# Kernel tuning notes

Hardware: AMD Instinct MI355X
Metric: run time of the kernel (lower is better)

The kernel has to match this reference:

```python
import jax, jax.numpy as jnp
import numpy as np

HIDDEN = 4096
NUM_HEADS = 32
HEAD_DIM = HIDDEN // NUM_HEADS  # 128
ROPE_THETA = 10000.0
SCALE = HEAD_DIM ** -0.5


def _apply_rope_neox(x, positions):
    # x: [B, S, H, D], positions: [B, S] int
    half = HEAD_DIM // 2
    inv_freq = 1.0 / (ROPE_THETA ** (jnp.arange(0, half, dtype=jnp.float32) / half))
    freqs = positions.astype(jnp.float32)[..., None] * inv_freq  # [B, S, half]
    cos = jnp.cos(freqs)[:, :, None, :]  # [B, S, 1, half]
    sin = jnp.sin(freqs)[:, :, None, :]
    x1, x2 = x[..., :half], x[..., half:]
    return jnp.concatenate([x1 * cos - x2 * sin, x2 * cos + x1 * sin], axis=-1)


def setup_inputs() -> dict:
    key = jax.random.key(0)
    k1, k2, k3, k4 = jax.random.split(key, 4)
    B, S = 2, 2048
    positions = jnp.broadcast_to(jnp.arange(S, dtype=jnp.int32), (B, S))
    hidden_states = jax.random.normal(k1, (B, S, HIDDEN), dtype=jnp.float32)
    w_qkv = jax.random.normal(k2, (HIDDEN, 3 * HIDDEN), dtype=jnp.float32) * (HIDDEN ** -0.5)
    b_qkv = jax.random.normal(k3, (3 * HIDDEN,), dtype=jnp.float32) * 0.02
    w_proj = jax.random.normal(k4, (HIDDEN, HIDDEN), dtype=jnp.float32) * (HIDDEN ** -0.5)
    return {"positions": positions, "hidden_states": hidden_states,
            "w_qkv": w_qkv, "b_qkv": b_qkv, "w_proj": w_proj}


def reference(positions, hidden_states, w_qkv, b_qkv, w_proj):
    B, S, _ = hidden_states.shape
    qkv = hidden_states @ w_qkv + b_qkv                     # [B, S, 3*HIDDEN]
    q, k, v = jnp.split(qkv, 3, axis=-1)
    q = q.reshape(B, S, NUM_HEADS, HEAD_DIM)
    k = k.reshape(B, S, NUM_HEADS, HEAD_DIM)
    v = v.reshape(B, S, NUM_HEADS, HEAD_DIM)
    q = _apply_rope_neox(q, positions)
    k = _apply_rope_neox(k, positions)
    scores = jnp.einsum('bqhd,bkhd->bhqk', q, k) * SCALE    # [B, H, S, S]
    causal = jnp.tril(jnp.ones((S, S), dtype=bool))
    scores = jnp.where(causal, scores, jnp.finfo(scores.dtype).min)
    probs = jax.nn.softmax(scores, axis=-1)
    attn = jnp.einsum('bhqk,bkhd->bqhd', probs, v).reshape(B, S, HIDDEN)
    return attn @ w_proj
```

## Files before the change

### kernel.cpp

```cpp
#include <hip/hip_runtime.h>
#include <hip/hip_bf16.h>
#include <math.h>

constexpr int B_   = 2;
constexpr int SEQ  = 2048;
constexpr int HID  = 4096;
constexpr int NH   = 32;
constexpr int HD   = 128;
constexpr float SCALE = 0.08838834764831845f;
constexpr size_t TEN = (size_t)B_ * NH * SEQ * HD;

typedef __attribute__((ext_vector_type(8))) __bf16 bf16x8;
typedef __attribute__((ext_vector_type(4))) float f32x4;

__device__ __forceinline__ ushort f2bf(float f) {
  uint u = __float_as_uint(f);
  return (ushort)((u + 0x7fffu + ((u >> 16) & 1u)) >> 16);
}
__device__ __forceinline__ float bfl(uint u) { return __uint_as_float(u << 16); }

__device__ __forceinline__ void gload16(const void* g, void* l) {
  __builtin_amdgcn_global_load_lds((__attribute__((address_space(1))) void*)(g),
                                   (__attribute__((address_space(3))) void*)(l),
                                   16, 0, 0);
}

__global__ __launch_bounds__(256) void conv_bf16(const float* __restrict__ in,
                                                 ushort* __restrict__ out) {
  const size_t i = ((size_t)blockIdx.x * 256 + threadIdx.x) * 8;
  float4 x = *(const float4*)(in + i);
  float4 y = *(const float4*)(in + i + 4);
  uint4 pk;
  pk.x = (uint)f2bf(x.x) | ((uint)f2bf(x.y) << 16);
  pk.y = (uint)f2bf(x.z) | ((uint)f2bf(x.w) << 16);
  pk.z = (uint)f2bf(y.x) | ((uint)f2bf(y.y) << 16);
  pk.w = (uint)f2bf(y.z) | ((uint)f2bf(y.w) << 16);
  *(uint4*)(out + i) = pk;
}

__global__ __launch_bounds__(256) void transp_bf16(const float* __restrict__ in,
                                                   ushort* __restrict__ out,
                                                   int R, int C) {
  __shared__ float t[32][33];
  const int tx = threadIdx.x & 31, ty = threadIdx.x >> 5;
  const int c0 = blockIdx.x * 32, r0 = blockIdx.y * 32;
  #pragma unroll
  for (int i = 0; i < 4; ++i)
    t[ty + 8*i][tx] = in[(size_t)(r0 + ty + 8*i) * C + c0 + tx];
  __syncthreads();
  #pragma unroll
  for (int i = 0; i < 4; ++i)
    out[(size_t)(c0 + ty + 8*i) * R + r0 + tx] = f2bf(t[tx][ty + 8*i]);
}

template<int MODE>
__global__ __launch_bounds__(256) void gemm_mfma(const ushort* __restrict__ A,
                                                 const ushort* __restrict__ Bt,
                                                 const float* __restrict__ bias,
                                                 void* __restrict__ outp,
                                                 int N, int K) {
  __shared__ __align__(16) ushort As[128 * 32];
  __shared__ __align__(16) ushort Bs[128 * 32];
  const int tid = threadIdx.x;
  const int wave = tid >> 6, lane = tid & 63;
  const int wr = wave >> 1, wc = wave & 1;
  const int m0 = blockIdx.y * 128, n0 = blockIdx.x * 128;

  f32x4 acc[4][4];
  #pragma unroll
  for (int i = 0; i < 4; ++i)
    #pragma unroll
    for (int j = 0; j < 4; ++j) acc[i][j] = (f32x4){0.f, 0.f, 0.f, 0.f};

  const int srow = 32 * wave + (lane >> 2);
  const int skq8 = (lane & 3) * 8;
  const ushort* Ag0 = A  + (size_t)(m0 + srow) * K + skq8;
  const ushort* Bg0 = Bt + (size_t)(n0 + srow) * K + skq8;
  char* AsB = (char*)As + wave * 2048;
  char* BsB = (char*)Bs + wave * 2048;

  const int fl  = lane & 15;
  const int kh8 = (lane >> 4) * 8;
  const ushort* Ar = As + (wr * 64 + fl) * 32 + kh8;
  const ushort* Br = Bs + (wc * 64 + fl) * 32 + kh8;

  for (int k0 = 0; k0 < K; k0 += 32) {
    __syncthreads();
    gload16(Ag0 + k0,          AsB);
    gload16(Ag0 + k0 + 16 * K, AsB + 1024);
    gload16(Bg0 + k0,          BsB);
    gload16(Bg0 + k0 + 16 * K, BsB + 1024);
    __syncthreads();
    bf16x8 a[4], b[4];
    #pragma unroll
    for (int m = 0; m < 4; ++m) a[m] = *(const bf16x8*)(Ar + m * 512);
    #pragma unroll
    for (int n = 0; n < 4; ++n) b[n] = *(const bf16x8*)(Br + n * 512);
    #pragma unroll
    for (int m = 0; m < 4; ++m)
      #pragma unroll
      for (int n = 0; n < 4; ++n)
        acc[m][n] = __builtin_amdgcn_mfma_f32_16x16x32_bf16(a[m], b[n], acc[m][n], 0, 0, 0);
  }

  const int rq4 = (lane >> 4) * 4;
  if (MODE == 0) {
    const int which = n0 >> 12;
    const int h     = (n0 >> 7) & 31;
    ushort* dst0 = (ushort*)outp + (size_t)which * TEN + (size_t)h * (SEQ * HD);
    #pragma unroll
    for (int n = 0; n < 4; ++n) {
      const int d = wc * 64 + n * 16 + fl;
      const float bv = bias[n0 + d];
      #pragma unroll
      for (int m = 0; m < 4; ++m) {
        const int rowb = m0 + wr * 64 + m * 16 + rq4;
        #pragma unroll
        for (int r = 0; r < 4; ++r) {
          const int t = rowb + r;
          const int b = t >> 11, s = t & 2047;
          dst0[(size_t)b * (NH * SEQ * HD) + (size_t)s * HD + d] = f2bf(acc[m][n][r] + bv);
        }
      }
    }
  } else {
    float* C = (float*)outp;
    #pragma unroll
    for (int n = 0; n < 4; ++n) {
      const int d = wc * 64 + n * 16 + fl;
      #pragma unroll
      for (int m = 0; m < 4; ++m) {
        const int rowb = m0 + wr * 64 + m * 16 + rq4;
        #pragma unroll
        for (int r = 0; r < 4; ++r)
          C[(size_t)(rowb + r) * N + n0 + d] = acc[m][n][r];
      }
    }
  }
}

__global__ __launch_bounds__(256) void rope_kernel(ushort* __restrict__ qbuf,
                                                   ushort* __restrict__ kbuf,
                                                   const int* __restrict__ positions) {
  const int idx = blockIdx.x * 256 + threadIdx.x;
  const int d  = idx & 63;
  const int s  = (idx >> 6) & 2047;
  const int bh = idx >> 17;
  const size_t off = ((size_t)bh * SEQ + s) * HD;
  const int pos = positions[(bh >> 5) * SEQ + s];
  const float invf = exp2f(-(float)d * 0.20762050593046014f);
  const float ang = (float)pos * invf;
  float sn, cs;
  sincosf(ang, &sn, &cs);
  {
    float x1 = bfl(qbuf[off + d]), x2 = bfl(qbuf[off + d + 64]);
    qbuf[off + d]      = f2bf((x1 * cs - x2 * sn) * SCALE);
    qbuf[off + d + 64] = f2bf((x2 * cs + x1 * sn) * SCALE);
  }
  {
    float x1 = bfl(kbuf[off + d]), x2 = bfl(kbuf[off + d + 64]);
    kbuf[off + d]      = f2bf(x1 * cs - x2 * sn);
    kbuf[off + d + 64] = f2bf(x2 * cs + x1 * sn);
  }
}

__global__ __launch_bounds__(256) void attn_mfma(const ushort* __restrict__ Q,
                                                 const ushort* __restrict__ K,
                                                 const ushort* __restrict__ V,
                                                 ushort* __restrict__ Out) {
  __shared__ __align__(16) ushort Ks[64 * 128];
  __shared__ __align__(16) ushort Vt[128 * 64];
  __shared__ __align__(16) ushort Pl[4 * 16 * 64];
  const int tid  = threadIdx.x;
  const int wave = tid >> 6, lane = tid & 63;
  const int fl = lane & 15, hh = lane >> 4;
  const int qs   = blockIdx.x * 64;
  const int qs_w = qs + wave * 16;
  const int bh   = blockIdx.y;
  const ushort* Qb = Q + (size_t)bh * SEQ * HD;
  const ushort* Kb = K + (size_t)bh * SEQ * HD;
  const ushort* Vb = V + (size_t)bh * SEQ * HD;

  bf16x8 qa[4];
  {
    const ushort* qrow = Qb + (size_t)(qs_w + fl) * HD + hh * 8;
    #pragma unroll
    for (int kk = 0; kk < 4; ++kk)
      qa[kk] = *(const bf16x8*)(qrow + 32 * kk);
  }

  f32x4 o_acc[8];
  #pragma unroll
  for (int dt = 0; dt < 8; ++dt) o_acc[dt] = (f32x4){0.f, 0.f, 0.f, 0.f};
  float mrow[4] = {-INFINITY, -INFINITY, -INFINITY, -INFINITY};
  float lrow[4] = {0.f, 0.f, 0.f, 0.f};

  char* KsC = (char*)Ks;
  char* VtC = (char*)Vt;
  ushort* Pw = Pl + wave * (16 * 64);

  const int nt = qs / 64 + 1;
  for (int jt = 0; jt < nt; ++jt) {
    const int j0 = jt * 64;
    __syncthreads();

    #pragma unroll
    for (int i = 0; i < 4; ++i) {
      const int seg = i * 4 + wave;
      const int row = 4 * seg + hh;
      const int gc  = fl ^ (row & 7);
      gload16(Kb + (size_t)(j0 + row) * HD + gc * 8, KsC + seg * 1024);
    }
    #pragma unroll
    for (int a = 0; a < 2; ++a) {
      const int idx   = tid + a * 256;
      const int chunk = idx & 15;
      const int pair  = idx >> 4;
      const int d0    = chunk * 8;
      uint4 v0 = *(const uint4*)(Vb + (size_t)(j0 + 2 * pair) * HD + d0);
      uint4 v1 = *(const uint4*)(Vb + (size_t)(j0 + 2 * pair + 1) * HD + d0);
      const ushort* u0 = (const ushort*)&v0;
      const ushort* u1 = (const ushort*)&v1;
      #pragma unroll
      for (int j = 0; j < 8; ++j) {
        const int d = d0 + j;
        const int byt = (d * 128 + pair * 4) ^ (((d >> 3) & 7) << 4);
        *(uint*)(VtC + byt) = (uint)u0[j] | ((uint)u1[j] << 16);
      }
    }
    __syncthreads();

    f32x4 sa[4];
    #pragma unroll
    for (int cc = 0; cc < 4; ++cc) sa[cc] = (f32x4){0.f, 0.f, 0.f, 0.f};
    #pragma unroll
    for (int cc = 0; cc < 4; ++cc) {
      const int row = fl + 16 * cc;
      const int rsw = row & 7;
      #pragma unroll
      for (int kk = 0; kk < 4; ++kk) {
        bf16x8 kb = *(const bf16x8*)(KsC + row * 256 + ((hh + 4 * kk) ^ rsw) * 16);
        sa[cc] = __builtin_amdgcn_mfma_f32_16x16x32_bf16(qa[kk], kb, sa[cc], 0, 0, 0);
      }
    }

    if (jt == nt - 1) {
      #pragma unroll
      for (int cc = 0; cc < 4; ++cc) {
        const int kv_g = j0 + fl + 16 * cc;
        #pragma unroll
        for (int r = 0; r < 4; ++r)
          if (kv_g > qs_w + 4 * hh + r) sa[cc][r] = -3.0e38f;
      }
    }

    float tmax[4], psum[4], resc[4];
    #pragma unroll
    for (int r = 0; r < 4; ++r) {
      float t = fmaxf(fmaxf(sa[0][r], sa[1][r]), fmaxf(sa[2][r], sa[3][r]));
      #pragma unroll
      for (int off = 1; off < 16; off <<= 1)
        t = fmaxf(t, __shfl_xor(t, off));
      tmax[r] = t;
    }
    #pragma unroll
    for (int r = 0; r < 4; ++r) {
      const float mnew = fmaxf(mrow[r], tmax[r]);
      resc[r] = __expf(mrow[r] - mnew);
      mrow[r] = mnew;
      float ps = 0.f;
      #pragma unroll
      for (int cc = 0; cc < 4; ++cc) {
        const float p = __expf(sa[cc][r] - mnew);
        sa[cc][r] = p;
        ps += p;
      }
      psum[r] = ps;
    }
    #pragma unroll
    for (int r = 0; r < 4; ++r) {
      float ps = psum[r];
      #pragma unroll
      for (int off = 1; off < 16; off <<= 1)
        ps += __shfl_xor(ps, off);
      lrow[r] = lrow[r] * resc[r] + ps;
    }
    #pragma unroll
    for (int dt = 0; dt < 8; ++dt)
      #pragma unroll
      for (int r = 0; r < 4; ++r) o_acc[dt][r] *= resc[r];

    #pragma unroll
    for (int cc = 0; cc < 4; ++cc) {
      const int kv = fl + 16 * cc;
      #pragma unroll
      for (int r = 0; r < 4; ++r) {
        const int q = 4 * hh + r;
        const int byt = q * 128 + (((kv >> 3) ^ (q & 7)) << 4) + (kv & 7) * 2;
        *(ushort*)((char*)Pw + byt) = f2bf(sa[cc][r]);
      }
    }

    #pragma unroll
    for (int chunk = 0; chunk < 2; ++chunk) {
      bf16x8 pa = *(const bf16x8*)((char*)Pw + fl * 128 +
                                   (((hh + 4 * chunk) ^ (fl & 7)) << 4));
      #pragma unroll
      for (int dt = 0; dt < 8; ++dt) {
        const int d = fl + 16 * dt;
        bf16x8 vbf = *(const bf16x8*)(VtC + ((d * 128 + hh * 16 + 64 * chunk) ^
                                             (((d >> 3) & 7) << 4)));
        o_acc[dt] = __builtin_amdgcn_mfma_f32_16x16x32_bf16(pa, vbf, o_acc[dt], 0, 0, 0);
      }
    }
  }

  float inv[4];
  #pragma unroll
  for (int r = 0; r < 4; ++r) inv[r] = 1.0f / lrow[r];
  const int b = bh >> 5, h = bh & 31;
  #pragma unroll
  for (int dt = 0; dt < 8; ++dt) {
    const int d = h * HD + dt * 16 + fl;
    #pragma unroll
    for (int r = 0; r < 4; ++r) {
      const int row_g = qs_w + 4 * hh + r;
      Out[((size_t)(b * SEQ + row_g)) * HID + d] = f2bf(o_acc[dt][r] * inv[r]);
    }
  }
}

extern "C" void kernel_launch(void* const* d_in, const int* in_sizes, int n_in,
                              void* d_out, int out_size, void* d_ws, size_t ws_size,
                              hipStream_t stream) {
  const int*   positions = (const int*)d_in[0];
  const float* hidden    = (const float*)d_in[1];
  const float* w_qkv     = (const float*)d_in[2];
  const float* b_qkv     = (const float*)d_in[3];
  const float* w_proj    = (const float*)d_in[4];
  float* out = (float*)d_out;

  ushort* ws16 = (ushort*)d_ws;
  ushort* qb = ws16;
  ushort* kb = ws16 + TEN;
  ushort* vb = ws16 + 2 * TEN;
  ushort* wT = ws16 + 3 * TEN;
  ushort* hA = ws16 + 3 * TEN + (size_t)(3 * HID) * HID;

  conv_bf16<<<8192, 256, 0, stream>>>(hidden, hA);
  transp_bf16<<<dim3(3 * HID / 32, HID / 32), 256, 0, stream>>>(w_qkv, wT, HID, 3 * HID);
  gemm_mfma<0><<<dim3(3 * HID / 128, 32), 256, 0, stream>>>(hA, wT, b_qkv, (void*)qb,
                                                            3 * HID, HID);
  rope_kernel<<<32768, 256, 0, stream>>>(qb, kb, positions);
  transp_bf16<<<dim3(HID / 32, HID / 32), 256, 0, stream>>>(w_proj, wT, HID, HID);
  attn_mfma<<<dim3(SEQ / 64, B_ * NH), 256, 0, stream>>>(qb, kb, vb, hA);
  gemm_mfma<1><<<dim3(HID / 128, 32), 256, 0, stream>>>(hA, wT, nullptr, (void*)out,
                                                        HID, HID);
}
```

Baseline: 1.960 ms.

## Double-buffer K/V tiles in attention and schedule longest causal blocks first

The attention kernel now double-buffers the K and V tiles in shared memory. The next tile's K is issued via async global-to-LDS loads and its V is loaded into registers before the current tile is computed, and V is transposed into LDS afterward. This overlaps global memory latency with MFMA work and drops one barrier per iteration. The grid is also reordered so the heaviest causal query blocks launch first, which reduces tail imbalance. The cost is twice the LDS for K/V (lower occupancy possible) and extra registers for the V prefetch.

```diff
diff --git a/kernel.cpp b/kernel.cpp
--- a/kernel.cpp
+++ b/kernel.cpp
@@ -168,15 +168,16 @@
                                                  const ushort* __restrict__ K,
                                                  const ushort* __restrict__ V,
                                                  ushort* __restrict__ Out) {
-  __shared__ __align__(16) ushort Ks[64 * 128];
-  __shared__ __align__(16) ushort Vt[128 * 64];
+  __shared__ __align__(16) ushort Ks[2][64 * 128];
+  __shared__ __align__(16) ushort Vt[2][128 * 64];
   __shared__ __align__(16) ushort Pl[4 * 16 * 64];
   const int tid  = threadIdx.x;
   const int wave = tid >> 6, lane = tid & 63;
   const int fl = lane & 15, hh = lane >> 4;
-  const int qs   = blockIdx.x * 64;
+  const int bh = blockIdx.x;
+  const int qi = (int)gridDim.y - 1 - (int)blockIdx.y;
+  const int qs   = qi * 64;
   const int qs_w = qs + wave * 16;
-  const int bh   = blockIdx.y;
   const ushort* Qb = Q + (size_t)bh * SEQ * HD;
   const ushort* Kb = K + (size_t)bh * SEQ * HD;
   const ushort* Vb = V + (size_t)bh * SEQ * HD;
@@ -195,15 +196,11 @@
   float mrow[4] = {-INFINITY, -INFINITY, -INFINITY, -INFINITY};
   float lrow[4] = {0.f, 0.f, 0.f, 0.f};
 
-  char* KsC = (char*)Ks;
-  char* VtC = (char*)Vt;
   ushort* Pw = Pl + wave * (16 * 64);
-
-  const int nt = qs / 64 + 1;
-  for (int jt = 0; jt < nt; ++jt) {
-    const int j0 = jt * 64;
-    __syncthreads();
-
+  uint4 vreg[4];
+
+  auto stageK = [&](int buf, int j0) {
+    char* KsC = (char*)Ks[buf];
     #pragma unroll
     for (int i = 0; i < 4; ++i) {
       const int seg = i * 4 + wave;
@@ -211,16 +208,26 @@
       const int gc  = fl ^ (row & 7);
       gload16(Kb + (size_t)(j0 + row) * HD + gc * 8, KsC + seg * 1024);
     }
+  };
+  auto loadV = [&](int j0) {
     #pragma unroll
     for (int a = 0; a < 2; ++a) {
-      const int idx   = tid + a * 256;
-      const int chunk = idx & 15;
-      const int pair  = idx >> 4;
-      const int d0    = chunk * 8;
-      uint4 v0 = *(const uint4*)(Vb + (size_t)(j0 + 2 * pair) * HD + d0);
-      uint4 v1 = *(const uint4*)(Vb + (size_t)(j0 + 2 * pair + 1) * HD + d0);
-      const ushort* u0 = (const ushort*)&v0;
-      const ushort* u1 = (const ushort*)&v1;
+      const int idx  = tid + a * 256;
+      const int d0   = (idx & 15) * 8;
+      const int pair = idx >> 4;
+      vreg[2*a]   = *(const uint4*)(Vb + (size_t)(j0 + 2*pair)     * HD + d0);
+      vreg[2*a+1] = *(const uint4*)(Vb + (size_t)(j0 + 2*pair + 1) * HD + d0);
+    }
+  };
+  auto writeV = [&](int buf) {
+    char* VtC = (char*)Vt[buf];
+    #pragma unroll
+    for (int a = 0; a < 2; ++a) {
+      const int idx  = tid + a * 256;
+      const int d0   = (idx & 15) * 8;
+      const int pair = idx >> 4;
+      const ushort* u0 = (const ushort*)&vreg[2*a];
+      const ushort* u1 = (const ushort*)&vreg[2*a+1];
       #pragma unroll
       for (int j = 0; j < 8; ++j) {
         const int d = d0 + j;
@@ -228,7 +235,22 @@
         *(uint*)(VtC + byt) = (uint)u0[j] | ((uint)u1[j] << 16);
       }
     }
-    __syncthreads();
+  };
+
+  const int nt = qi + 1;
+  stageK(0, 0);
+  loadV(0);
+  writeV(0);
+  __syncthreads();
+
+  int cur = 0;
+  for (int jt = 0; jt < nt; ++jt) {
+    const int j0 = jt * 64;
+    const bool more = (jt + 1 < nt);
+    if (more) { stageK(cur ^ 1, j0 + 64); loadV(j0 + 64); }
+
+    char* KsC = (char*)Ks[cur];
+    char* VtC = (char*)Vt[cur];
 
     f32x4 sa[4];
     #pragma unroll
@@ -313,6 +335,10 @@
         o_acc[dt] = __builtin_amdgcn_mfma_f32_16x16x32_bf16(pa, vbf, o_acc[dt], 0, 0, 0);
       }
     }
+
+    if (more) writeV(cur ^ 1);
+    __syncthreads();
+    cur ^= 1;
   }
 
   float inv[4];
@@ -353,7 +379,7 @@
                                                             3 * HID, HID);
   rope_kernel<<<32768, 256, 0, stream>>>(qb, kb, positions);
   transp_bf16<<<dim3(HID / 32, HID / 32), 256, 0, stream>>>(w_proj, wT, HID, HID);
-  attn_mfma<<<dim3(SEQ / 64, B_ * NH), 256, 0, stream>>>(qb, kb, vb, hA);
+  attn_mfma<<<dim3(B_ * NH, SEQ / 64), 256, 0, stream>>>(qb, kb, vb, hA);
   gemm_mfma<1><<<dim3(HID / 128, 32), 256, 0, stream>>>(hA, wT, nullptr, (void*)out,
                                                         HID, HID);
 }
```

Result: faster. 1.600 ms (-18.3%).
